# Kernel optimization log

Measured on AMD Instinct MI355X. Metric: run time of the kernel, lower is better.

The kernel has to match this reference:

```python
import jax, jax.numpy as jnp
import numpy as np

B, T, V, E, H, N = 8, 128, 32000, 128, 256, 20
SHARPEN = 5.0
EPS = 1e-8  # torch cosine_similarity eps


def setup_inputs() -> dict:
    key = jax.random.key(0)
    ks = jax.random.split(key, 8)
    g = lambda k, shape, scale: (jax.random.normal(k, shape, dtype=jnp.float32) * scale)
    return {
        "x_ids": jax.random.randint(ks[0], (B, T), 0, V),
        "emb": g(ks[1], (V, E), 0.02),                 # nn.Embedding weight
        "W_i": g(ks[2], (H, E), E ** -0.5),            # rnn_i weight (no bias)
        "W_h": g(ks[3], (H, H), H ** -0.5),            # rnn_h weight
        "W_fc": g(ks[4], (V, 2 * H), (2 * H) ** -0.5), # fc -> vocab (softmaxed)
        "W_ops": g(ks[5], (3, 2 * H), (2 * H) ** -0.5),
        "W_choose": g(ks[6], (2, 2 * H), (2 * H) ** -0.5),
        "sharp": jnp.array([SHARPEN], dtype=jnp.float32),
    }


def _l2norm(x, eps=1e-12):
    # F.normalize(x, dim=-1)
    n = jnp.linalg.norm(x, axis=-1, keepdims=True)
    return x / jnp.maximum(n, eps)


def reference(x_ids, emb, W_i, W_h, W_fc, W_ops, W_choose, sharp):
    x = emb[x_ids]                                   # [B,T,E]
    # pre-normalize vocab rows for cosine-sim readout (clamped like torch)
    emb_cn = emb / jnp.maximum(jnp.linalg.norm(emb, axis=1, keepdims=True), EPS)
    sh = sharp[0]

    stack0 = jnp.full((B, N, E), 0.001, dtype=x.dtype)      # zero_offset + 0.001
    ptr0 = jnp.zeros((B, N), x.dtype).at[:, 0].set(1.0)     # pointer at slot 0
    h0 = jnp.zeros((B, H), x.dtype)

    def step(carry, xi):
        h, stack, ptr = carry
        ri = _l2norm(xi) @ W_i.T                     # rnn_i(normalize(x_t))
        h = jnp.tanh(ri + h @ W_h.T)
        hm = 1.0 - jax.nn.relu(h)
        hmod = jnp.concatenate([hm, hm], axis=1)     # [B,2H]
        # GumbelSoftmax(temp=1, hard=False) -> deterministic softmax (no noise)
        ops = jax.nn.softmax(hmod @ W_ops.T, axis=1)  # [B,3]
        push, pop, nop = ops[:, 0], ops[:, 1], ops[:, 2]
        # --- differentiable stack push/pop/nop ---
        pop_val = jnp.einsum('bn,bne->be', ptr, stack)      # soft read at pointer
        p_push = jnp.roll(ptr, 1, axis=1)
        p_pop = jnp.roll(ptr, -1, axis=1)
        new_ptr = push[:, None] * p_push + pop[:, None] * p_pop + nop[:, None] * ptr
        new_ptr = jnp.clip(new_ptr, EPS) ** sh              # sharpen
        new_ptr = new_ptr / jnp.sum(new_ptr, axis=1, keepdims=True)
        w = (push[:, None] * p_push)[:, :, None]            # write weight [B,N,1]
        new_stack = stack * (1.0 - w) + w * xi[:, None, :]
        # --- readout ---
        semantic = jax.nn.softmax(hmod @ W_fc.T, axis=1)    # [B,V]
        pv_n = pop_val / jnp.maximum(
            jnp.linalg.norm(pop_val, axis=1, keepdims=True), EPS)
        syntactic = pv_n @ emb_cn.T                          # cosine sim [B,V]
        choice = jax.nn.softmax(hmod @ W_choose.T, axis=1)   # [B,2]
        out = choice[:, 0:1] * semantic + choice[:, 1:2] * syntactic
        return (h, new_stack, new_ptr), out

    _, outs = jax.lax.scan(step, (h0, stack0, ptr0), jnp.swapaxes(x, 0, 1))
    return jnp.swapaxes(outs, 0, 1)  # [B,T,V]
```

## Files before the change

### kernel.cpp

```cpp
#include <hip/hip_runtime.h>
#include <hip/hip_bf16.h>
#include <stdint.h>

#define T_ 128
#define B_ 8
#define V_ 32000
#define E_ 128
#define H_ 256
#define N_ 20
#define M_ 1024
#define PIT 264
#define PIT2 136
#define NCH2 1000

typedef __attribute__((ext_vector_type(8))) short short8;
typedef __attribute__((ext_vector_type(4))) float f32x4;
typedef unsigned short ushort;

static __device__ __forceinline__ ushort f2bf_u(float f) {
  __hip_bfloat16 h = __float2bfloat16(f);
  return *reinterpret_cast<ushort*>(&h);
}

__global__ void whT_k(const float* __restrict__ Wh, float* __restrict__ whT) {
  int idx = blockIdx.x*256 + threadIdx.x;
  int i = idx >> 8, j = idx & 255;
  whT[j*H_ + i] = Wh[i*H_ + j];
}

__global__ void wit_k(const float* __restrict__ Wi, float* __restrict__ WiT) {
  int idx = blockIdx.x*256 + threadIdx.x;
  if (idx < H_*E_) {
    int i = idx >> 7, e = idx & (E_-1);
    WiT[e*H_ + i] = Wi[idx];
  }
}

__global__ void embn_k(const float* __restrict__ emb, ushort* __restrict__ embnb) {
  int v = blockIdx.x, l = threadIdx.x;
  float e0 = emb[v*E_ + l];
  float e1 = emb[v*E_ + 64 + l];
  float ss = e0*e0 + e1*e1;
  #pragma unroll
  for (int off = 32; off >= 1; off >>= 1) ss += __shfl_xor(ss, off);
  float inv = 1.f / fmaxf(sqrtf(ss), 1e-8f);
  embnb[v*E_ + l]      = f2bf_u(e0*inv);
  embnb[v*E_ + 64 + l] = f2bf_u(e1*inv);
}

__global__ void foldfc_k(const float* __restrict__ Wfc, ushort* __restrict__ Wfcb) {
  int idx = blockIdx.x*256 + threadIdx.x;
  int n = idx >> 8, k = idx & 255;
  Wfcb[idx] = f2bf_u(Wfc[n*2*H_ + k] + Wfc[n*2*H_ + H_ + k]);
}

__global__ __launch_bounds__(256) void ri_k(const int* __restrict__ x_ids,
    const float* __restrict__ emb, const float* __restrict__ WiT,
    float* __restrict__ RI)
{
  __shared__ float xn[E_];
  __shared__ float red[2];
  int r = blockIdx.x, tid = threadIdx.x;
  int id = x_ids[r];
  float v = 0.f;
  if (tid < E_) v = emb[id*E_ + tid];
  float ss = v*v;
  if (tid < E_) {
    #pragma unroll
    for (int off = 32; off >= 1; off >>= 1) ss += __shfl_xor(ss, off);
    if ((tid & 63) == 0) red[tid >> 6] = ss;
  }
  __syncthreads();
  float inv = 1.f / fmaxf(sqrtf(red[0] + red[1]), 1e-12f);
  if (tid < E_) xn[tid] = v*inv;
  __syncthreads();
  float s = 0.f;
  for (int e = 0; e < E_; ++e) s += xn[e]*WiT[e*H_ + tid];
  RI[r*H_ + tid] = s;
}

__global__ __launch_bounds__(512, 1) void chain_k(
    const float* __restrict__ whT, const float* __restrict__ RI,
    float* __restrict__ HMf, ushort* __restrict__ HMb)
{
  __shared__ __align__(8) float hlds[H_];
  __shared__ float hred[H_];
  const int b = blockIdx.x, tid = threadIdx.x;
  const int q = tid >> 8, i = tid & 255;

  float wreg[128];
  #pragma unroll
  for (int u = 0; u < 128; ++u) wreg[u] = whT[(q*128 + u)*H_ + i];

  if (tid < H_) hlds[tid] = 0.f;
  __syncthreads();

  for (int t = 0; t < T_; ++t) {
    const int r = b*T_ + t;
    float ri = RI[r*H_ + i];
    const float2* h2 = reinterpret_cast<const float2*>(hlds);
    float p0 = 0.f, p1 = 0.f, p2 = 0.f, p3 = 0.f;
    #pragma unroll
    for (int u = 0; u < 16; ++u) {
      float2 ha = h2[q*64 + u*4 + 0];
      float2 hb = h2[q*64 + u*4 + 1];
      float2 hc = h2[q*64 + u*4 + 2];
      float2 hd = h2[q*64 + u*4 + 3];
      p0 += wreg[u*8+0]*ha.x + wreg[u*8+1]*ha.y;
      p1 += wreg[u*8+2]*hb.x + wreg[u*8+3]*hb.y;
      p2 += wreg[u*8+4]*hc.x + wreg[u*8+5]*hc.y;
      p3 += wreg[u*8+6]*hd.x + wreg[u*8+7]*hd.y;
    }
    float p = (p0 + p1) + (p2 + p3);
    if (q == 1) hred[i] = p;
    __syncthreads();
    if (q == 0) {
      float s = ri + p + hred[i];
      float hn = tanhf(s);
      hlds[i] = hn;
      float hm = 1.f - fmaxf(hn, 0.f);
      HMf[r*H_ + i] = hm;
      HMb[r*H_ + i] = f2bf_u(hm);
    }
    __syncthreads();
  }
}

__global__ void dots_k(const float* __restrict__ HMf,
    const float* __restrict__ W_ops, const float* __restrict__ W_ch,
    float* __restrict__ OPS, float* __restrict__ CH)
{
  int r = blockIdx.x, l = threadIdx.x;
  float4 hm4 = reinterpret_cast<const float4*>(HMf + (size_t)r*H_)[l];
  float d[5];
  #pragma unroll
  for (int k = 0; k < 3; ++k) {
    float w0 = W_ops[k*2*H_ + 4*l+0] + W_ops[k*2*H_ + H_ + 4*l+0];
    float w1 = W_ops[k*2*H_ + 4*l+1] + W_ops[k*2*H_ + H_ + 4*l+1];
    float w2 = W_ops[k*2*H_ + 4*l+2] + W_ops[k*2*H_ + H_ + 4*l+2];
    float w3 = W_ops[k*2*H_ + 4*l+3] + W_ops[k*2*H_ + H_ + 4*l+3];
    d[k] = hm4.x*w0 + hm4.y*w1 + hm4.z*w2 + hm4.w*w3;
  }
  #pragma unroll
  for (int k = 0; k < 2; ++k) {
    float w0 = W_ch[k*2*H_ + 4*l+0] + W_ch[k*2*H_ + H_ + 4*l+0];
    float w1 = W_ch[k*2*H_ + 4*l+1] + W_ch[k*2*H_ + H_ + 4*l+1];
    float w2 = W_ch[k*2*H_ + 4*l+2] + W_ch[k*2*H_ + H_ + 4*l+2];
    float w3 = W_ch[k*2*H_ + 4*l+3] + W_ch[k*2*H_ + H_ + 4*l+3];
    d[3+k] = hm4.x*w0 + hm4.y*w1 + hm4.z*w2 + hm4.w*w3;
  }
  #pragma unroll
  for (int off = 32; off >= 1; off >>= 1)
    #pragma unroll
    for (int k = 0; k < 5; ++k) d[k] += __shfl_xor(d[k], off);
  if (l == 0) {
    float mx = fmaxf(d[0], fmaxf(d[1], d[2]));
    float e0 = expf(d[0]-mx), e1 = expf(d[1]-mx), e2 = expf(d[2]-mx);
    float oi = 1.f/(e0+e1+e2);
    OPS[r*4+0] = e0*oi; OPS[r*4+1] = e1*oi; OPS[r*4+2] = e2*oi;
    float cm = fmaxf(d[3], d[4]);
    float f0 = expf(d[3]-cm), f1 = expf(d[4]-cm);
    float ci = 1.f/(f0+f1);
    CH[r*2] = f0*ci; CH[r*2+1] = f1*ci;
  }
}

__global__ __launch_bounds__(64) void ptrw_k(const float* __restrict__ OPS,
    const float* __restrict__ sharp, float2* __restrict__ PTRW)
{
  __shared__ float ops_s[T_*4];
  const int b = blockIdx.x, l = threadIdx.x;
  for (int m = l; m < T_*4; m += 64) ops_s[m] = OPS[(size_t)b*T_*4 + m];
  const float sh = sharp[0];
  float ptr = (l == 0) ? 1.f : 0.f;
  const int lp = (l + N_ - 1) % N_;
  const int ln = (l + 1) % N_;
  for (int t = 0; t < T_; ++t) {
    float push = ops_s[t*4+0], pop = ops_s[t*4+1], nop = ops_s[t*4+2];
    float pp = __shfl(ptr, lp);
    float po = __shfl(ptr, ln);
    float w = push*pp;
    float raw = w + pop*po + nop*ptr;
    float np = 0.f;
    if (l < N_) np = exp2f(sh * log2f(fmaxf(raw, 1e-8f)));
    float ssum = np;
    #pragma unroll
    for (int off = 1; off < 32; off <<= 1) ssum += __shfl_xor(ssum, off);
    if (l < N_) {
      PTRW[(size_t)(b*T_ + t)*N_ + l] = make_float2(ptr, w);
      ptr = np / ssum;
    }
  }
}

__global__ __launch_bounds__(128) void pv_k(const int* __restrict__ x_ids,
    const float* __restrict__ emb, const float2* __restrict__ PTRW,
    float* __restrict__ PV)
{
  __shared__ float2 pw_s[T_*N_];
  __shared__ int ids_s[T_];
  const int b = blockIdx.x, e = threadIdx.x;
  for (int m = e; m < T_*N_; m += 128) pw_s[m] = PTRW[(size_t)b*T_*N_ + m];
  if (e < T_) ids_s[e] = x_ids[b*T_ + e];
  __syncthreads();
  float stck[N_];
  #pragma unroll
  for (int n = 0; n < N_; ++n) stck[n] = 0.001f;
  float xi_c = emb[(size_t)ids_s[0]*E_ + e];
  for (int t = 0; t < T_; ++t) {
    float xi_n = (t+1 < T_) ? emb[(size_t)ids_s[t+1]*E_ + e] : 0.f;
    float pv = 0.f;
    #pragma unroll
    for (int n = 0; n < N_; ++n) {
      float2 pw = pw_s[t*N_ + n];
      pv += pw.x * stck[n];
      stck[n] += pw.y * (xi_c - stck[n]);
    }
    PV[(size_t)(b*T_ + t)*E_ + e] = pv;
    xi_c = xi_n;
  }
}

__global__ void pvn_k(const float* __restrict__ PV, ushort* __restrict__ PVNb) {
  int r = blockIdx.x, l = threadIdx.x;
  float a = PV[(size_t)r*E_ + l];
  float c = PV[(size_t)r*E_ + 64 + l];
  float ss = a*a + c*c;
  #pragma unroll
  for (int off = 32; off >= 1; off >>= 1) ss += __shfl_xor(ss, off);
  float inv = 1.f / fmaxf(sqrtf(ss), 1e-8f);
  PVNb[(size_t)r*E_ + l]      = f2bf_u(a*inv);
  PVNb[(size_t)r*E_ + 64 + l] = f2bf_u(c*inv);
}

__global__ __launch_bounds__(256) void stats2_k(const ushort* __restrict__ HMb,
    const ushort* __restrict__ Wfcb, float* __restrict__ SS)
{
  __shared__ __align__(16) ushort As[64*PIT];
  __shared__ __align__(16) ushort Bs[64*PIT];
  const int tid = threadIdx.x;
  const int Rb = blockIdx.y*64, Cb = blockIdx.x*64;
  const uint4* srcA = (const uint4*)(HMb  + (size_t)Rb*H_);
  const uint4* srcB = (const uint4*)(Wfcb + (size_t)Cb*H_);
  #pragma unroll
  for (int it = 0; it < 8; ++it) {
    int idx = it*256 + tid, row = idx >> 5, c = idx & 31;
    *(uint4*)&As[row*PIT + c*8] = srcA[row*32 + c];
    *(uint4*)&Bs[row*PIT + c*8] = srcB[row*32 + c];
  }
  __syncthreads();

  const int wave = tid >> 6, lane = tid & 63;
  const int wr = wave >> 1, wc = wave & 1;
  const int lr = lane & 15, g = lane >> 4;
  f32x4 acc[2][2] = {};
  const ushort* Ab = &As[(wr*32 + lr)*PIT + g*8];
  const ushort* Bb = &Bs[(wc*32 + lr)*PIT + g*8];
  #pragma unroll
  for (int ks = 0; ks < 8; ++ks) {
    short8 a0 = *(const short8*)(Ab + ks*32);
    short8 a1 = *(const short8*)(Ab + 16*PIT + ks*32);
    short8 b0 = *(const short8*)(Bb + ks*32);
    short8 b1 = *(const short8*)(Bb + 16*PIT + ks*32);
    acc[0][0] = __builtin_amdgcn_mfma_f32_16x16x32_bf16(a0, b0, acc[0][0], 0, 0, 0);
    acc[0][1] = __builtin_amdgcn_mfma_f32_16x16x32_bf16(a0, b1, acc[0][1], 0, 0, 0);
    acc[1][0] = __builtin_amdgcn_mfma_f32_16x16x32_bf16(a1, b0, acc[1][0], 0, 0, 0);
    acc[1][1] = __builtin_amdgcn_mfma_f32_16x16x32_bf16(a1, b1, acc[1][1], 0, 0, 0);
  }
  const int chunk = blockIdx.x*2 + wc;
  #pragma unroll
  for (int mi = 0; mi < 2; ++mi)
    #pragma unroll
    for (int r = 0; r < 4; ++r) {
      float s = expf(acc[mi][0][r]) + expf(acc[mi][1][r]);
      #pragma unroll
      for (int off = 1; off < 16; off <<= 1) s += __shfl_xor(s, off);
      if (lr == 0) SS[(size_t)(Rb + wr*32 + mi*16 + g*4 + r)*NCH2 + chunk] = s;
    }
}

__global__ void reduce2_k(const float* __restrict__ SS, float* __restrict__ MS) {
  int row = blockIdx.x, l = threadIdx.x;
  float s = 0.f;
  for (int c = l; c < NCH2; c += 64) s += SS[(size_t)row*NCH2 + c];
  #pragma unroll
  for (int off = 32; off >= 1; off >>= 1) s += __shfl_xor(s, off);
  if (l == 0) MS[row] = 1.f/s;
}

__global__ __launch_bounds__(256) void final2_k(const ushort* __restrict__ HMb,
    const ushort* __restrict__ Wfcb, const ushort* __restrict__ PVNb,
    const ushort* __restrict__ embnb, const float* __restrict__ MS,
    const float* __restrict__ CH, float* __restrict__ out)
{
  __shared__ __align__(16) ushort As[64*PIT];
  __shared__ __align__(16) ushort Bs[64*PIT];
  const int tid = threadIdx.x;
  const int Rb = blockIdx.y*64, Cb = blockIdx.x*64;
  const int wave = tid >> 6, lane = tid & 63;
  const int wr = wave >> 1, wc = wave & 1;
  const int lr = lane & 15, g = lane >> 4;

  {
    const uint4* srcA = (const uint4*)(HMb  + (size_t)Rb*H_);
    const uint4* srcB = (const uint4*)(Wfcb + (size_t)Cb*H_);
    #pragma unroll
    for (int it = 0; it < 8; ++it) {
      int idx = it*256 + tid, row = idx >> 5, c = idx & 31;
      *(uint4*)&As[row*PIT + c*8] = srcA[row*32 + c];
      *(uint4*)&Bs[row*PIT + c*8] = srcB[row*32 + c];
    }
  }
  __syncthreads();
  f32x4 accL[2][2] = {};
  {
    const ushort* Ab = &As[(wr*32 + lr)*PIT + g*8];
    const ushort* Bb = &Bs[(wc*32 + lr)*PIT + g*8];
    #pragma unroll
    for (int ks = 0; ks < 8; ++ks) {
      short8 a0 = *(const short8*)(Ab + ks*32);
      short8 a1 = *(const short8*)(Ab + 16*PIT + ks*32);
      short8 b0 = *(const short8*)(Bb + ks*32);
      short8 b1 = *(const short8*)(Bb + 16*PIT + ks*32);
      accL[0][0] = __builtin_amdgcn_mfma_f32_16x16x32_bf16(a0, b0, accL[0][0], 0, 0, 0);
      accL[0][1] = __builtin_amdgcn_mfma_f32_16x16x32_bf16(a0, b1, accL[0][1], 0, 0, 0);
      accL[1][0] = __builtin_amdgcn_mfma_f32_16x16x32_bf16(a1, b0, accL[1][0], 0, 0, 0);
      accL[1][1] = __builtin_amdgcn_mfma_f32_16x16x32_bf16(a1, b1, accL[1][1], 0, 0, 0);
    }
  }
  __syncthreads();

  {
    const uint4* srcA = (const uint4*)(PVNb  + (size_t)Rb*E_);
    const uint4* srcB = (const uint4*)(embnb + (size_t)Cb*E_);
    #pragma unroll
    for (int it = 0; it < 4; ++it) {
      int idx = it*256 + tid, row = idx >> 4, c = idx & 15;
      *(uint4*)&As[row*PIT2 + c*8] = srcA[row*16 + c];
      *(uint4*)&Bs[row*PIT2 + c*8] = srcB[row*16 + c];
    }
  }
  __syncthreads();
  f32x4 accS[2][2] = {};
  {
    const ushort* Ab = &As[(wr*32 + lr)*PIT2 + g*8];
    const ushort* Bb = &Bs[(wc*32 + lr)*PIT2 + g*8];
    #pragma unroll
    for (int ks = 0; ks < 4; ++ks) {
      short8 a0 = *(const short8*)(Ab + ks*32);
      short8 a1 = *(const short8*)(Ab + 16*PIT2 + ks*32);
      short8 b0 = *(const short8*)(Bb + ks*32);
      short8 b1 = *(const short8*)(Bb + 16*PIT2 + ks*32);
      accS[0][0] = __builtin_amdgcn_mfma_f32_16x16x32_bf16(a0, b0, accS[0][0], 0, 0, 0);
      accS[0][1] = __builtin_amdgcn_mfma_f32_16x16x32_bf16(a0, b1, accS[0][1], 0, 0, 0);
      accS[1][0] = __builtin_amdgcn_mfma_f32_16x16x32_bf16(a1, b0, accS[1][0], 0, 0, 0);
      accS[1][1] = __builtin_amdgcn_mfma_f32_16x16x32_bf16(a1, b1, accS[1][1], 0, 0, 0);
    }
  }

  #pragma unroll
  for (int mi = 0; mi < 2; ++mi)
    #pragma unroll
    for (int r = 0; r < 4; ++r) {
      int row = Rb + wr*32 + mi*16 + g*4 + r;
      float Si = MS[row];
      float c0 = CH[row*2], c1 = CH[row*2+1];
      float v0 = c0*expf(accL[mi][0][r])*Si + c1*accS[mi][0][r];
      float v1 = c0*expf(accL[mi][1][r])*Si + c1*accS[mi][1][r];
      size_t base = (size_t)row*V_ + Cb + wc*32 + lr;
      out[base]      = v0;
      out[base + 16] = v1;
    }
}

extern "C" void kernel_launch(void* const* d_in, const int* in_sizes, int n_in,
                              void* d_out, int out_size, void* d_ws, size_t ws_size,
                              hipStream_t stream) {
  const int*   x_ids = (const int*)d_in[0];
  const float* emb   = (const float*)d_in[1];
  const float* W_i   = (const float*)d_in[2];
  const float* W_h   = (const float*)d_in[3];
  const float* W_fc  = (const float*)d_in[4];
  const float* W_ops = (const float*)d_in[5];
  const float* W_ch  = (const float*)d_in[6];
  const float* sharp = (const float*)d_in[7];
  float* out = (float*)d_out;

  float* ws    = (float*)d_ws;
  float*  whT  = ws;
  float*  WiT  = whT + 65536;
  float*  RI   = WiT + 32768;
  float*  CH   = RI + 262144;
  float*  MS   = CH + 2048;
  float*  SS   = MS + 1024;
  float*  HMf  = SS + 1024000;
  float*  OPS  = HMf + 262144;
  float*  PV   = OPS + 4096;
  float2* PTRW = (float2*)(PV + 131072);
  float*  fend = PV + 131072 + 40960;
  ushort* HMb   = (ushort*)fend;
  ushort* PVNb  = HMb + 262144;
  ushort* Wfcb  = PVNb + 131072;
  ushort* embnb = Wfcb + 8192000;

  whT_k  <<<H_*H_/256, 256, 0, stream>>>(W_h, whT);
  wit_k  <<<(H_*E_ + 255)/256, 256, 0, stream>>>(W_i, WiT);
  embn_k <<<V_, 64, 0, stream>>>(emb, embnb);
  foldfc_k<<<V_*H_/256, 256, 0, stream>>>(W_fc, Wfcb);
  ri_k   <<<M_, 256, 0, stream>>>(x_ids, emb, WiT, RI);
  chain_k<<<B_, 512, 0, stream>>>(whT, RI, HMf, HMb);
  dots_k <<<M_, 64, 0, stream>>>(HMf, W_ops, W_ch, OPS, CH);
  ptrw_k <<<B_, 64, 0, stream>>>(OPS, sharp, PTRW);
  pv_k   <<<B_, 128, 0, stream>>>(x_ids, emb, PTRW, PV);
  pvn_k  <<<M_, 64, 0, stream>>>(PV, PVNb);
  stats2_k<<<dim3(V_/64, M_/64), 256, 0, stream>>>(HMb, Wfcb, SS);
  reduce2_k<<<M_, 64, 0, stream>>>(SS, MS);
  final2_k<<<dim3(V_/64, M_/64), 256, 0, stream>>>(HMb, Wfcb, PVNb, embnb, MS, CH, out);
}
```

Before: 446.3 us.

## Run RNN recurrence with one thread per hidden unit and double-buffered state

The sequential tanh recurrence kernel now uses 256 threads, each holding a full 256-entry column of W_h in registers, instead of splitting the dot product across two thread halves. This removes the partial-sum exchange through shared memory and one of the two barriers per timestep. The hidden state is double-buffered and read as float4, and the next step's input projection is prefetched. In exchange, each thread does twice the FMA work and holds 256 weight registers, which risks spills or low occupancy on a serial critical path.

```diff
diff --git a/kernel.cpp b/kernel.cpp
--- a/kernel.cpp
+++ b/kernel.cpp
@@ -79,49 +79,42 @@
   RI[r*H_ + tid] = s;
 }
 
-__global__ __launch_bounds__(512, 1) void chain_k(
+__global__ __launch_bounds__(256, 1) void chain_k(
     const float* __restrict__ whT, const float* __restrict__ RI,
     float* __restrict__ HMf, ushort* __restrict__ HMb)
 {
-  __shared__ __align__(8) float hlds[H_];
-  __shared__ float hred[H_];
-  const int b = blockIdx.x, tid = threadIdx.x;
-  const int q = tid >> 8, i = tid & 255;
-
-  float wreg[128];
-  #pragma unroll
-  for (int u = 0; u < 128; ++u) wreg[u] = whT[(q*128 + u)*H_ + i];
-
-  if (tid < H_) hlds[tid] = 0.f;
-  __syncthreads();
+  __shared__ __align__(16) float hbuf[2][H_];
+  const int b = blockIdx.x, i = threadIdx.x;
+
+  float wreg[256];
+  #pragma unroll
+  for (int u = 0; u < 256; ++u) wreg[u] = whT[u*H_ + i];
+
+  hbuf[0][i] = 0.f;
+  __syncthreads();
+  float ri_c = RI[(size_t)b*T_*H_ + i];
 
   for (int t = 0; t < T_; ++t) {
     const int r = b*T_ + t;
-    float ri = RI[r*H_ + i];
-    const float2* h2 = reinterpret_cast<const float2*>(hlds);
+    float ri_n = 0.f;
+    if (t+1 < T_) ri_n = RI[(size_t)(r+1)*H_ + i];
+    const float4* h4 = reinterpret_cast<const float4*>(hbuf[t & 1]);
     float p0 = 0.f, p1 = 0.f, p2 = 0.f, p3 = 0.f;
     #pragma unroll
     for (int u = 0; u < 16; ++u) {
-      float2 ha = h2[q*64 + u*4 + 0];
-      float2 hb = h2[q*64 + u*4 + 1];
-      float2 hc = h2[q*64 + u*4 + 2];
-      float2 hd = h2[q*64 + u*4 + 3];
-      p0 += wreg[u*8+0]*ha.x + wreg[u*8+1]*ha.y;
-      p1 += wreg[u*8+2]*hb.x + wreg[u*8+3]*hb.y;
-      p2 += wreg[u*8+4]*hc.x + wreg[u*8+5]*hc.y;
-      p3 += wreg[u*8+6]*hd.x + wreg[u*8+7]*hd.y;
-    }
-    float p = (p0 + p1) + (p2 + p3);
-    if (q == 1) hred[i] = p;
-    __syncthreads();
-    if (q == 0) {
-      float s = ri + p + hred[i];
-      float hn = tanhf(s);
-      hlds[i] = hn;
-      float hm = 1.f - fmaxf(hn, 0.f);
-      HMf[r*H_ + i] = hm;
-      HMb[r*H_ + i] = f2bf_u(hm);
-    }
+      float4 xa = h4[u*4+0], xb = h4[u*4+1], xc = h4[u*4+2], xd = h4[u*4+3];
+      p0 += wreg[u*16+ 0]*xa.x + wreg[u*16+ 1]*xa.y + wreg[u*16+ 2]*xa.z + wreg[u*16+ 3]*xa.w;
+      p1 += wreg[u*16+ 4]*xb.x + wreg[u*16+ 5]*xb.y + wreg[u*16+ 6]*xb.z + wreg[u*16+ 7]*xb.w;
+      p2 += wreg[u*16+ 8]*xc.x + wreg[u*16+ 9]*xc.y + wreg[u*16+10]*xc.z + wreg[u*16+11]*xc.w;
+      p3 += wreg[u*16+12]*xd.x + wreg[u*16+13]*xd.y + wreg[u*16+14]*xd.z + wreg[u*16+15]*xd.w;
+    }
+    float s = ri_c + (p0 + p1) + (p2 + p3);
+    float hn = tanhf(s);
+    hbuf[(t+1) & 1][i] = hn;
+    float hm = 1.f - fmaxf(hn, 0.f);
+    HMf[(size_t)r*H_ + i] = hm;
+    HMb[(size_t)r*H_ + i] = f2bf_u(hm);
+    ri_c = ri_n;
     __syncthreads();
   }
 }
@@ -408,7 +401,7 @@
   embn_k <<<V_, 64, 0, stream>>>(emb, embnb);
   foldfc_k<<<V_*H_/256, 256, 0, stream>>>(W_fc, Wfcb);
   ri_k   <<<M_, 256, 0, stream>>>(x_ids, emb, WiT, RI);
-  chain_k<<<B_, 512, 0, stream>>>(whT, RI, HMf, HMb);
+  chain_k<<<B_, 256, 0, stream>>>(whT, RI, HMf, HMb);
   dots_k <<<M_, 64, 0, stream>>>(HMf, W_ops, W_ch, OPS, CH);
   ptrw_k <<<B_, 64, 0, stream>>>(OPS, sharp, PTRW);
   pv_k   <<<B_, 128, 0, stream>>>(x_ids, emb, PTRW, PV);
```

Result: slower. 518.1 us (+16.1%).
